# Optimization experiments

Measured on AMD Instinct MI355X. Metric: run time of the kernel, lower is better.

## Reference

```python
import jax, jax.numpy as jnp
import numpy as np

SL, BS, HS = 2048, 2, 1024
FFN, E, TOP_K = 4096, 8, 2


def setup_inputs() -> dict:
    key = jax.random.key(0)
    k1, k2, k3, k4, k5 = jax.random.split(key, 5)
    x = jax.random.normal(k1, (SL, BS, HS), dtype=jnp.float32)
    expert_weights = jax.random.uniform(k2, (SL * BS, TOP_K), dtype=jnp.float32)
    expert_indices = jax.random.randint(k3, (SL * BS, TOP_K), 0, E, dtype=jnp.int32)
    w1 = jax.random.normal(k4, (E, HS, FFN), dtype=jnp.float32) * 0.02
    w2 = jax.random.normal(k5, (E, FFN, HS), dtype=jnp.float32) * 0.02
    return {"x": x, "expert_weights": expert_weights,
            "expert_indices": expert_indices, "w1": w1, "w2": w2}


def reference(x, expert_weights, expert_indices, w1, w2):
    # Dropless MoE: y[t] = sum_k expert_weights[t,k] * MLP_{expert_indices[t,k]}(x[t])
    # Equivalent to megablocks sort/gather/grouped-GEMM/scatter pipeline, expressed
    # as a fixed loop over the (small) expert axis with masked weighted combine.
    sl, bs, hs = x.shape
    xf = x.reshape(-1, hs)                       # [T, hs]
    ew = expert_weights.reshape(xf.shape[0], -1)  # [T, k]
    ei = expert_indices.reshape(xf.shape[0], -1)  # [T, k]
    out = jnp.zeros_like(xf)
    for e in range(w1.shape[0]):
        h = jnp.dot(jax.nn.gelu(jnp.dot(xf, w1[e])), w2[e])   # [T, hs]
        coef = jnp.sum(jnp.where(ei == e, ew, 0.0), axis=-1)  # [T]
        out = out + coef[:, None] * h
    return out.reshape(sl, bs, hs)
```

## Files before the change

kernel.cpp:

```cpp
#include <hip/hip_runtime.h>
#include <stdint.h>

#define SLEN 2048
#define BSZ  2
#define HSZ  1024
#define FFND 4096
#define NEXP 8
#define TOPK 2
#define NTOK (SLEN*BSZ)
#define NSLOT (NTOK*TOPK)

#define BM 128
#define BN 128
#define BK 32
#define SPLITK 2
#define KS (FFND / SPLITK)

using short8 = __attribute__((ext_vector_type(8))) short;
using f32x4  = __attribute__((ext_vector_type(4))) float;

typedef __attribute__((address_space(1))) const unsigned int gu32;
typedef __attribute__((address_space(3))) unsigned int lu32;

__device__ inline void async_copy16(const void* g, void* l){
  __builtin_amdgcn_global_load_lds((gu32*)g, (lu32*)l, 16, 0, 0);
}

__device__ inline unsigned short f2bf(float f){
  unsigned u = __builtin_bit_cast(unsigned, f);
  u += 0x7FFFu + ((u >> 16) & 1u);
  return (unsigned short)(u >> 16);
}

__device__ inline float gelu_tanh(float x){
  float u = 0.7978845608028654f * (x + 0.044715f * x * x * x);
  return 0.5f * x * (1.0f + tanhf(u));
}


__global__ void k_count(const int* __restrict__ ei, int* __restrict__ counts){
  int i = blockIdx.x * blockDim.x + threadIdx.x;
  if (i < NSLOT) atomicAdd(&counts[ei[i]], 1);
}

__global__ void k_scan(const int* __restrict__ counts, int* __restrict__ offsets,
                       int* __restrict__ fill){
  if (threadIdx.x == 0 && blockIdx.x == 0){
    int acc = 0;
    for (int e = 0; e < NEXP; e++){ offsets[e] = acc; fill[e] = acc; acc += counts[e]; }
  }
}

__global__ void k_assign(const int* __restrict__ ei, const float* __restrict__ ew,
                         int* __restrict__ fill, int* __restrict__ rowT,
                         float* __restrict__ rowC){
  int i = blockIdx.x * blockDim.x + threadIdx.x;
  if (i < NSLOT){
    int e = ei[i];
    int slot = atomicAdd(&fill[e], 1);
    rowT[slot] = i >> 1;
    rowC[slot] = ew[i];
  }
}

__global__ void k_gather(const float* __restrict__ x, const int* __restrict__ rowT,
                         unsigned short* __restrict__ Xg){
  int slot = blockIdx.x;
  int t = rowT[slot];
  int c = threadIdx.x * 4;
  float4 v = *(const float4*)(x + (size_t)t * HSZ + c);
  ushort4 o;
  o.x = f2bf(v.x); o.y = f2bf(v.y); o.z = f2bf(v.z); o.w = f2bf(v.w);
  *(ushort4*)(Xg + (size_t)slot * HSZ + c) = o;
}

__global__ __launch_bounds__(256) void k_transpose2(const float* __restrict__ w1,
                                                    const float* __restrict__ w2,
                                                    unsigned short* __restrict__ Wt1,
                                                    unsigned short* __restrict__ Wt2){
  __shared__ unsigned short tile[64][65];
  const int tid = threadIdx.x;
  int z = blockIdx.y;
  const float* src; unsigned short* dst; int R, C, r0, c0;
  if (z < NEXP){
    src = w1 + (size_t)z * HSZ * FFND; dst = Wt1 + (size_t)z * HSZ * FFND;
    R = HSZ; C = FFND;
    c0 = (blockIdx.x & 63) * 64; r0 = (blockIdx.x >> 6) * 64;
  } else {
    z -= NEXP;
    src = w2 + (size_t)z * FFND * HSZ; dst = Wt2 + (size_t)z * FFND * HSZ;
    R = FFND; C = HSZ;
    c0 = (blockIdx.x & 15) * 64; r0 = (blockIdx.x >> 4) * 64;
  }
  #pragma unroll
  for (int p = 0; p < 4; p++){
    int r  = p * 16 + (tid >> 4);
    int cc = (tid & 15) * 4;
    float4 v = *(const float4*)(src + (size_t)(r0 + r) * C + c0 + cc);
    tile[r][cc]   = f2bf(v.x);
    tile[r][cc+1] = f2bf(v.y);
    tile[r][cc+2] = f2bf(v.z);
    tile[r][cc+3] = f2bf(v.w);
  }
  __syncthreads();
  #pragma unroll
  for (int p = 0; p < 4; p++){
    int c  = p * 16 + (tid >> 4);
    int rr = (tid & 15) * 4;
    ushort4 o;
    o.x = tile[rr][c]; o.y = tile[rr+1][c]; o.z = tile[rr+2][c]; o.w = tile[rr+3][c];
    *(ushort4*)(dst + (size_t)(c0 + c) * R + r0 + rr) = o;
  }
}

__device__ inline void gemm_core(const unsigned short* __restrict__ Ag, int lda, int rows,
                                 const unsigned short* __restrict__ Bg, int ldb, int K,
                                 unsigned short* As, unsigned short* Bs,
                                 f32x4 acc[4][4])
{
  const int tid  = threadIdx.x;
  const int lane = tid & 63;
  const int wid  = tid >> 6;
  const int wm   = (wid & 1) * 64;
  const int wn   = (wid >> 1) * 64;
  const int q    = lane >> 4;
  const int l16  = lane & 15;

  for (int k0 = 0; k0 < K; k0 += BK){
    #pragma unroll
    for (int p = 0; p < 2; p++){
      int c  = (wid * 2 + p) * 64 + lane;
      int r  = c >> 2;
      int kp = (c & 3) * 8;
      int ra = min(r, rows - 1);
      async_copy16(Ag + (size_t)ra * lda + k0 + kp, As + (wid * 2 + p) * 512);
      async_copy16(Bg + (size_t)r  * ldb + k0 + kp, Bs + (wid * 2 + p) * 512);
    }
    __syncthreads();

    short8 af[4], bfr[4];
    #pragma unroll
    for (int i = 0; i < 4; i++)
      af[i] = *(const short8*)(As + (wm + i * 16 + l16) * BK + q * 8);
    #pragma unroll
    for (int j = 0; j < 4; j++)
      bfr[j] = *(const short8*)(Bs + (wn + j * 16 + l16) * BK + q * 8);

    #pragma unroll
    for (int i = 0; i < 4; i++)
      #pragma unroll
      for (int j = 0; j < 4; j++)
        acc[i][j] = __builtin_amdgcn_mfma_f32_16x16x32_bf16(af[i], bfr[j], acc[i][j], 0, 0, 0);
    __syncthreads();
  }
}

__global__ __launch_bounds__(256) void k_gemm1(const unsigned short* __restrict__ Xg,
                                               const unsigned short* __restrict__ Wt1,
                                               unsigned short* __restrict__ H,
                                               const int* __restrict__ counts,
                                               const int* __restrict__ offsets)
{
  __shared__ unsigned short smem[BM * BK + BN * BK];
  unsigned short* As = smem;
  unsigned short* Bs = smem + BM * BK;
  const int e    = blockIdx.z;
  const int cnt  = counts[e];
  const int mblk = blockIdx.y;
  if (mblk * BM >= cnt) return;
  const int n0   = blockIdx.x * BN;
  const int row0 = offsets[e] + mblk * BM;
  const int rows = min(BM, cnt - mblk * BM);

  f32x4 acc[4][4] = {};
  gemm_core(Xg + (size_t)row0 * HSZ, HSZ, rows,
            Wt1 + (size_t)e * HSZ * FFND + (size_t)n0 * HSZ, HSZ, HSZ, As, Bs, acc);

  const int lane = threadIdx.x & 63, wid = threadIdx.x >> 6;
  const int wm = (wid & 1) * 64, wn = (wid >> 1) * 64;
  const int q = lane >> 4, l16 = lane & 15;

  unsigned short* scr = smem + wid * (16 * 68);
  #pragma unroll
  for (int i = 0; i < 4; i++){
    #pragma unroll
    for (int j = 0; j < 4; j++)
      #pragma unroll
      for (int r = 0; r < 4; r++)
        scr[(q * 4 + r) * 68 + j * 16 + l16] = f2bf(gelu_tanh(acc[i][j][r]));
    #pragma unroll
    for (int p = 0; p < 2; p++){
      int rr = p * 8 + (lane >> 3);
      int cc = (lane & 7) * 8;
      short8 v = *(const short8*)(scr + rr * 68 + cc);
      int grow = wm + i * 16 + rr;
      if (grow < rows)
        *(short8*)(H + (size_t)(row0 + grow) * FFND + n0 + wn + cc) = v;
    }
  }
}

__global__ __launch_bounds__(256) void k_gemm2(const unsigned short* __restrict__ H,
                                               const unsigned short* __restrict__ Wt2,
                                               float* __restrict__ out,
                                               const int* __restrict__ counts,
                                               const int* __restrict__ offsets,
                                               const int* __restrict__ rowT,
                                               const float* __restrict__ rowC)
{
  __shared__ unsigned short As[BM * BK];
  __shared__ unsigned short Bs[BN * BK];
  const int e    = blockIdx.z >> 1;
  const int s    = blockIdx.z & 1;
  const int cnt  = counts[e];
  const int mblk = blockIdx.y;
  if (mblk * BM >= cnt) return;
  const int n0   = blockIdx.x * BN;
  const int row0 = offsets[e] + mblk * BM;
  const int rows = min(BM, cnt - mblk * BM);

  f32x4 acc[4][4] = {};
  gemm_core(H + (size_t)row0 * FFND + (size_t)s * KS, FFND, rows,
            Wt2 + (size_t)e * FFND * HSZ + (size_t)n0 * FFND + (size_t)s * KS,
            FFND, KS, As, Bs, acc);

  const int lane = threadIdx.x & 63, wid = threadIdx.x >> 6;
  const int wm = (wid & 1) * 64, wn = (wid >> 1) * 64;
  const int q = lane >> 4, l16 = lane & 15;
  #pragma unroll
  for (int i = 0; i < 4; i++)
    #pragma unroll
    for (int j = 0; j < 4; j++)
      #pragma unroll
      for (int r = 0; r < 4; r++){
        int row = wm + i * 16 + q * 4 + r;
        if (row < rows){
          int g = row0 + row;
          int col = wn + j * 16 + l16;
          atomicAdd(out + (size_t)rowT[g] * HSZ + n0 + col, rowC[g] * acc[i][j][r]);
        }
      }
}

static inline size_t align_up(size_t v, size_t a){ return (v + a - 1) & ~(a - 1); }

extern "C" void kernel_launch(void* const* d_in, const int* in_sizes, int n_in,
                              void* d_out, int out_size, void* d_ws, size_t ws_size,
                              hipStream_t stream) {
  const float* x  = (const float*)d_in[0];
  const float* ew = (const float*)d_in[1];
  const int*   ei = (const int*)d_in[2];
  const float* w1 = (const float*)d_in[3];
  const float* w2 = (const float*)d_in[4];
  float* out = (float*)d_out;

  char* base = (char*)d_ws;
  size_t off = 0;
  int* counts  = (int*)(base + off); off += 64;
  int* fill    = (int*)(base + off); off += 64;
  int* offsets = (int*)(base + off); off = align_up(off + 64, 4096);
  int* rowT    = (int*)(base + off); off += (size_t)NSLOT * 4;
  float* rowC  = (float*)(base + off); off = align_up(off + (size_t)NSLOT * 4, 1 << 20);
  unsigned short* Xg  = (unsigned short*)(base + off); off = align_up(off + (size_t)NSLOT * HSZ * 2, 1 << 20);
  unsigned short* H   = (unsigned short*)(base + off); off = align_up(off + (size_t)NSLOT * FFND * 2, 1 << 20);
  unsigned short* Wt1 = (unsigned short*)(base + off); off = align_up(off + (size_t)NEXP * HSZ * FFND * 2, 1 << 20);
  unsigned short* Wt2 = (unsigned short*)(base + off); off += (size_t)NEXP * FFND * HSZ * 2;
  (void)ws_size;

  hipMemsetAsync(d_out, 0, (size_t)out_size * sizeof(float), stream);
  hipMemsetAsync(counts, 0, 64, stream);

  k_count <<<NSLOT / 256, 256, 0, stream>>>(ei, counts);
  k_scan  <<<1, 64, 0, stream>>>(counts, offsets, fill);
  k_assign<<<NSLOT / 256, 256, 0, stream>>>(ei, ew, fill, rowT, rowC);
  k_gather<<<NSLOT, 256, 0, stream>>>(x, rowT, Xg);

  k_transpose2<<<dim3(1024, 2 * NEXP), 256, 0, stream>>>(w1, w2, Wt1, Wt2);

  k_gemm1<<<dim3(FFND / BN, 64, NEXP), 256, 0, stream>>>(Xg, Wt1, H, counts, offsets);
  k_gemm2<<<dim3(HSZ / BN, 64, NEXP * SPLITK), 256, 0, stream>>>(H, Wt2, out, counts, offsets, rowT, rowC);
}
```

Baseline: 700.6 us.

## Fuse routing kernels, double BK, and replace split-K gemm2 with narrower N tiles

Merges the count/scan/assign routing kernels into one single-block kernel using shared-memory histogram, removing two launches and a memset. The GEMM core now uses BK=64 split into two 32-wide LDS halves, halving barrier count per K. gemm2 drops split-K in favor of 64-wide N tiles, halving atomic adds into the output, at the cost of less reuse of the A tile per block. LDS usage doubles per block, which may reduce occupancy.

Result: faster. 629.9 us (-10.1%).

```diff
diff --git a/kernel.cpp b/kernel.cpp
--- a/kernel.cpp
+++ b/kernel.cpp
@@ -11,10 +11,7 @@
 #define NSLOT (NTOK*TOPK)
 
 #define BM 128
-#define BN 128
-#define BK 32
-#define SPLITK 2
-#define KS (FFND / SPLITK)
+#define BK 64
 
 using short8 = __attribute__((ext_vector_type(8))) short;
 using f32x4  = __attribute__((ext_vector_type(4))) float;
@@ -37,27 +34,35 @@
   return 0.5f * x * (1.0f + tanhf(u));
 }
 
-
-__global__ void k_count(const int* __restrict__ ei, int* __restrict__ counts){
-  int i = blockIdx.x * blockDim.x + threadIdx.x;
-  if (i < NSLOT) atomicAdd(&counts[ei[i]], 1);
-}
-
-__global__ void k_scan(const int* __restrict__ counts, int* __restrict__ offsets,
-                       int* __restrict__ fill){
-  if (threadIdx.x == 0 && blockIdx.x == 0){
+__global__ __launch_bounds__(1024) void k_route(const int* __restrict__ ei,
+                                                const float* __restrict__ ew,
+                                                int* __restrict__ counts,
+                                                int* __restrict__ offsets,
+                                                int* __restrict__ rowT,
+                                                float* __restrict__ rowC){
+  __shared__ int hist[NEXP];
+  __shared__ int fill[NEXP];
+  const int tid = threadIdx.x;
+  if (tid < NEXP) hist[tid] = 0;
+  __syncthreads();
+  int myE[NSLOT / 1024];
+  #pragma unroll
+  for (int p = 0; p < NSLOT / 1024; p++){
+    myE[p] = ei[tid + p * 1024];
+    atomicAdd(&hist[myE[p]], 1);
+  }
+  __syncthreads();
+  if (tid == 0){
     int acc = 0;
-    for (int e = 0; e < NEXP; e++){ offsets[e] = acc; fill[e] = acc; acc += counts[e]; }
-  }
-}
-
-__global__ void k_assign(const int* __restrict__ ei, const float* __restrict__ ew,
-                         int* __restrict__ fill, int* __restrict__ rowT,
-                         float* __restrict__ rowC){
-  int i = blockIdx.x * blockDim.x + threadIdx.x;
-  if (i < NSLOT){
-    int e = ei[i];
-    int slot = atomicAdd(&fill[e], 1);
+    for (int e = 0; e < NEXP; e++){
+      offsets[e] = acc; counts[e] = hist[e]; fill[e] = acc; acc += hist[e];
+    }
+  }
+  __syncthreads();
+  #pragma unroll
+  for (int p = 0; p < NSLOT / 1024; p++){
+    int i = tid + p * 1024;
+    int slot = atomicAdd(&fill[myE[p]], 1);
     rowT[slot] = i >> 1;
     rowC[slot] = ew[i];
   }
@@ -113,44 +118,60 @@
   }
 }
 
+template<int JF>
 __device__ inline void gemm_core(const unsigned short* __restrict__ Ag, int lda, int rows,
                                  const unsigned short* __restrict__ Bg, int ldb, int K,
                                  unsigned short* As, unsigned short* Bs,
-                                 f32x4 acc[4][4])
+                                 f32x4 acc[4][JF])
 {
+  const int BNt  = 32 * JF;
   const int tid  = threadIdx.x;
   const int lane = tid & 63;
   const int wid  = tid >> 6;
   const int wm   = (wid & 1) * 64;
-  const int wn   = (wid >> 1) * 64;
+  const int wn   = (wid >> 1) * (16 * JF);
   const int q    = lane >> 4;
   const int l16  = lane & 15;
+  const int rl   = lane >> 2;
+  const int cl   = lane & 3;
 
   for (int k0 = 0; k0 < K; k0 += BK){
     #pragma unroll
-    for (int p = 0; p < 2; p++){
-      int c  = (wid * 2 + p) * 64 + lane;
-      int r  = c >> 2;
-      int kp = (c & 3) * 8;
-      int ra = min(r, rows - 1);
-      async_copy16(Ag + (size_t)ra * lda + k0 + kp, As + (wid * 2 + p) * 512);
-      async_copy16(Bg + (size_t)r  * ldb + k0 + kp, Bs + (wid * 2 + p) * 512);
+    for (int h = 0; h < 2; h++)
+      #pragma unroll
+      for (int p = 0; p < 2; p++){
+        int r0 = wid * 32 + p * 16;
+        int gr = min(r0 + rl, rows - 1);
+        async_copy16(Ag + (size_t)gr * lda + k0 + h * 32 + cl * 8,
+                     As + h * (BM * 32) + r0 * 32);
+      }
+    #pragma unroll
+    for (int h = 0; h < 2; h++)
+      #pragma unroll
+      for (int p = 0; p < BNt / 64; p++){
+        int r0 = wid * (BNt / 4) + p * 16;
+        async_copy16(Bg + (size_t)(r0 + rl) * ldb + k0 + h * 32 + cl * 8,
+                     Bs + h * (BNt * 32) + r0 * 32);
+      }
+    __syncthreads();
+
+    short8 af[4][2], bfr[JF][2];
+    #pragma unroll
+    for (int h = 0; h < 2; h++){
+      #pragma unroll
+      for (int i = 0; i < 4; i++)
+        af[i][h] = *(const short8*)(As + h * (BM * 32) + (wm + i * 16 + l16) * 32 + q * 8);
+      #pragma unroll
+      for (int j = 0; j < JF; j++)
+        bfr[j][h] = *(const short8*)(Bs + h * (BNt * 32) + (wn + j * 16 + l16) * 32 + q * 8);
     }
-    __syncthreads();
-
-    short8 af[4], bfr[4];
-    #pragma unroll
-    for (int i = 0; i < 4; i++)
-      af[i] = *(const short8*)(As + (wm + i * 16 + l16) * BK + q * 8);
-    #pragma unroll
-    for (int j = 0; j < 4; j++)
-      bfr[j] = *(const short8*)(Bs + (wn + j * 16 + l16) * BK + q * 8);
-
-    #pragma unroll
-    for (int i = 0; i < 4; i++)
-      #pragma unroll
-      for (int j = 0; j < 4; j++)
-        acc[i][j] = __builtin_amdgcn_mfma_f32_16x16x32_bf16(af[i], bfr[j], acc[i][j], 0, 0, 0);
+    #pragma unroll
+    for (int h = 0; h < 2; h++)
+      #pragma unroll
+      for (int i = 0; i < 4; i++)
+        #pragma unroll
+        for (int j = 0; j < JF; j++)
+          acc[i][j] = __builtin_amdgcn_mfma_f32_16x16x32_bf16(af[i][h], bfr[j][h], acc[i][j], 0, 0, 0);
     __syncthreads();
   }
 }
@@ -161,20 +182,20 @@
                                                const int* __restrict__ counts,
                                                const int* __restrict__ offsets)
 {
-  __shared__ unsigned short smem[BM * BK + BN * BK];
+  __shared__ unsigned short smem[BM * BK + 128 * BK];
   unsigned short* As = smem;
   unsigned short* Bs = smem + BM * BK;
   const int e    = blockIdx.z;
   const int cnt  = counts[e];
   const int mblk = blockIdx.y;
   if (mblk * BM >= cnt) return;
-  const int n0   = blockIdx.x * BN;
+  const int n0   = blockIdx.x * 128;
   const int row0 = offsets[e] + mblk * BM;
   const int rows = min(BM, cnt - mblk * BM);
 
   f32x4 acc[4][4] = {};
-  gemm_core(Xg + (size_t)row0 * HSZ, HSZ, rows,
-            Wt1 + (size_t)e * HSZ * FFND + (size_t)n0 * HSZ, HSZ, HSZ, As, Bs, acc);
+  gemm_core<4>(Xg + (size_t)row0 * HSZ, HSZ, rows,
+               Wt1 + (size_t)e * HSZ * FFND + (size_t)n0 * HSZ, HSZ, HSZ, As, Bs, acc);
 
   const int lane = threadIdx.x & 63, wid = threadIdx.x >> 6;
   const int wm = (wid & 1) * 64, wn = (wid >> 1) * 64;
@@ -209,28 +230,26 @@
                                                const float* __restrict__ rowC)
 {
   __shared__ unsigned short As[BM * BK];
-  __shared__ unsigned short Bs[BN * BK];
-  const int e    = blockIdx.z >> 1;
-  const int s    = blockIdx.z & 1;
+  __shared__ unsigned short Bs[64 * BK];
+  const int e    = blockIdx.z;
   const int cnt  = counts[e];
   const int mblk = blockIdx.y;
   if (mblk * BM >= cnt) return;
-  const int n0   = blockIdx.x * BN;
+  const int n0   = blockIdx.x * 64;
   const int row0 = offsets[e] + mblk * BM;
   const int rows = min(BM, cnt - mblk * BM);
 
-  f32x4 acc[4][4] = {};
-  gemm_core(H + (size_t)row0 * FFND + (size_t)s * KS, FFND, rows,
-            Wt2 + (size_t)e * FFND * HSZ + (size_t)n0 * FFND + (size_t)s * KS,
-            FFND, KS, As, Bs, acc);
+  f32x4 acc[4][2] = {};
+  gemm_core<2>(H + (size_t)row0 * FFND, FFND, rows,
+               Wt2 + (size_t)e * FFND * HSZ + (size_t)n0 * FFND, FFND, FFND, As, Bs, acc);
 
   const int lane = threadIdx.x & 63, wid = threadIdx.x >> 6;
-  const int wm = (wid & 1) * 64, wn = (wid >> 1) * 64;
+  const int wm = (wid & 1) * 64, wn = (wid >> 1) * 32;
   const int q = lane >> 4, l16 = lane & 15;
   #pragma unroll
   for (int i = 0; i < 4; i++)
     #pragma unroll
-    for (int j = 0; j < 4; j++)
+    for (int j = 0; j < 2; j++)
       #pragma unroll
       for (int r = 0; r < 4; r++){
         int row = wm + i * 16 + q * 4 + r;
@@ -257,7 +276,6 @@
   char* base = (char*)d_ws;
   size_t off = 0;
   int* counts  = (int*)(base + off); off += 64;
-  int* fill    = (int*)(base + off); off += 64;
   int* offsets = (int*)(base + off); off = align_up(off + 64, 4096);
   int* rowT    = (int*)(base + off); off += (size_t)NSLOT * 4;
   float* rowC  = (float*)(base + off); off = align_up(off + (size_t)NSLOT * 4, 1 << 20);
@@ -268,15 +286,12 @@
   (void)ws_size;
 
   hipMemsetAsync(d_out, 0, (size_t)out_size * sizeof(float), stream);
-  hipMemsetAsync(counts, 0, 64, stream);
-
-  k_count <<<NSLOT / 256, 256, 0, stream>>>(ei, counts);
-  k_scan  <<<1, 64, 0, stream>>>(counts, offsets, fill);
-  k_assign<<<NSLOT / 256, 256, 0, stream>>>(ei, ew, fill, rowT, rowC);
+
+  k_route <<<1, 1024, 0, stream>>>(ei, ew, counts, offsets, rowT, rowC);
   k_gather<<<NSLOT, 256, 0, stream>>>(x, rowT, Xg);
 
   k_transpose2<<<dim3(1024, 2 * NEXP), 256, 0, stream>>>(w1, w2, Wt1, Wt2);
 
-  k_gemm1<<<dim3(FFND / BN, 64, NEXP), 256, 0, stream>>>(Xg, Wt1, H, counts, offsets);
-  k_gemm2<<<dim3(HSZ / BN, 64, NEXP * SPLITK), 256, 0, stream>>>(H, Wt2, out, counts, offsets, rowT, rowC);
-}
+  k_gemm1<<<dim3(FFND / 128, 64, NEXP), 256, 0, stream>>>(Xg, Wt1, H, counts, offsets);
+  k_gemm2<<<dim3(HSZ / 64, 64, NEXP), 256, 0, stream>>>(H, Wt2, out, counts, offsets, rowT, rowC);
+}
```
